# Kernel tuning notes

Measured on AMD Instinct MI355X. Metric: run time of the kernel, lower is better.

Reference implementation:

```python
import jax, jax.numpy as jnp
import numpy as np

B, S, H, P = 4, 4096, 1024, 10

def setup_inputs() -> dict:
    key = jax.random.key(0)
    k1, k2, k3, k4, k5 = jax.random.split(key, 5)
    return {
        "query": jax.random.normal(k1, (B, S, H), dtype=jnp.float32),
        "key": jax.random.normal(k2, (B, S, H), dtype=jnp.float32),
        "value": jax.random.normal(k3, (B, S, H), dtype=jnp.float32),
        "prefix_k": jax.random.normal(k4, (P, H), dtype=jnp.float32),
        "prefix_v": jax.random.normal(k5, (P, H), dtype=jnp.float32),
    }

def reference(query, key, value, prefix_k, prefix_v):
    # Broadcast learned prefix over batch and concat ahead of real K/V.
    b = query.shape[0]
    pk = jnp.broadcast_to(prefix_k[None], (b,) + prefix_k.shape)  # [B, P, H]
    pv = jnp.broadcast_to(prefix_v[None], (b,) + prefix_v.shape)
    k_all = jnp.concatenate([pk, key], axis=1)    # [B, P+S, H]
    v_all = jnp.concatenate([pv, value], axis=1)  # [B, P+S, H]
    # Raw (unscaled, unmasked) attention, exactly as the torch module does.
    scores = jnp.einsum("bqh,bkh->bqk", query, k_all)  # [B, S, P+S]
    attn = jax.nn.softmax(scores, axis=-1)
    return jnp.einsum("bqk,bkh->bqh", attn, v_all)     # [B, S, H]
```

## Files before the change

kernel.cpp:

```cpp
#include <hip/hip_runtime.h>
#include <cstdint>
#include <cstddef>

#define BB 4
#define SS 4096
#define HH 1024
#define PP 10
#define LL 4106
#define NTILES 129
#define CHUNKS_PB (NTILES * 4096)
#define TILE_ELEMS (4096 * 8)
#define LOG2E 1.44269504088896f

typedef __attribute__((ext_vector_type(8))) _Float16 half8v;
typedef __attribute__((ext_vector_type(4))) float float4v;

union hu16 { _Float16 h; unsigned short u; };

__device__ __forceinline__ half8v cvt8h(float4v f0, float4v f1) {
  half8v h;
  h[0] = (_Float16)f0[0]; h[1] = (_Float16)f0[1];
  h[2] = (_Float16)f0[2]; h[3] = (_Float16)f0[3];
  h[4] = (_Float16)f1[0]; h[5] = (_Float16)f1[1];
  h[6] = (_Float16)f1[2]; h[7] = (_Float16)f1[3];
  return h;
}
__device__ __forceinline__ unsigned pack2h(float a, float b) {
  hu16 x, y; x.h = (_Float16)a; y.h = (_Float16)b;
  return (unsigned)x.u | ((unsigned)y.u << 16);
}

template<int C>
__device__ __forceinline__ float dppf(float x) {
  return __int_as_float(
      __builtin_amdgcn_update_dpp(0, __float_as_int(x), C, 0xF, 0xF, true));
}
__device__ __forceinline__ float row16_max(float x) {
  x = fmaxf(x, dppf<0xB1>(x));
  x = fmaxf(x, dppf<0x4E>(x));
  x = fmaxf(x, dppf<0x140>(x));
  x = fmaxf(x, dppf<0x141>(x));
  return x;
}
__device__ __forceinline__ float row16_sum(float x) {
  x += dppf<0xB1>(x);
  x += dppf<0x4E>(x);
  x += dppf<0x140>(x);
  x += dppf<0x141>(x);
  return x;
}

#define LGKM_BAR() do { \
  asm volatile("s_waitcnt lgkmcnt(0)" ::: "memory"); \
  __builtin_amdgcn_s_barrier(); \
  asm volatile("" ::: "memory"); } while (0)

__global__ __launch_bounds__(256) void conv_k(const float* __restrict__ prefix_k,
                                              const float* __restrict__ key,
                                              _Float16* __restrict__ kp) {
  const int b = blockIdx.y;
  const int id = blockIdx.x * 256 + threadIdx.x;
  const int li = id & 15, g = (id >> 4) & 3, ktp = (id >> 6) & 31,
            nt = (id >> 11) & 1, it = id >> 12;
  const int n = it * 32 + nt * 16 + li;
  const int d = ktp * 32 + g * 8;
  float4v f0 = {0.f, 0.f, 0.f, 0.f}, f1 = {0.f, 0.f, 0.f, 0.f};
  if (n < LL) {
    const float* src = (n < PP) ? prefix_k + (size_t)n * HH + d
                                : key + ((size_t)b * SS + (n - PP)) * HH + d;
    f0 = *(const float4v*)src; f1 = *(const float4v*)(src + 4);
  }
  *(half8v*)(kp + ((size_t)b * CHUNKS_PB + id) * 8) = cvt8h(f0, f1);
}

__global__ __launch_bounds__(256) void conv_v(const float* __restrict__ prefix_v,
                                              const float* __restrict__ value,
                                              _Float16* __restrict__ vp) {
  const int b = blockIdx.y;
  const int id = blockIdx.x * 256 + threadIdx.x;
  const int d = id & 1023, g = (id >> 10) & 3, it = id >> 12;
  const int nb = it * 32 + g * 8;
  half8v h;
  #pragma unroll
  for (int j = 0; j < 8; ++j) {
    int n = nb + j;
    float f = 0.f;
    if (n < LL)
      f = (n < PP) ? prefix_v[(size_t)n * HH + d]
                   : value[((size_t)b * SS + (n - PP)) * HH + d];
    h[j] = (_Float16)f;
  }
  *(half8v*)(vp + ((size_t)b * CHUNKS_PB + id) * 8) = h;
}

template<int PATH>
__global__ __launch_bounds__(512, 2) void attn_fused(
    const float* __restrict__ q,
    const float* __restrict__ key,
    const float* __restrict__ value,
    const float* __restrict__ prefix_k,
    const float* __restrict__ prefix_v,
    const _Float16* __restrict__ kp,
    const _Float16* __restrict__ vp,
    float* __restrict__ out)
{
  __shared__ __align__(16) float sbuf0[8][32][36];
  __shared__ __align__(16) float sbuf1[8][32][36];
  __shared__ __align__(16) unsigned short Pl0[32][40];
  __shared__ __align__(16) unsigned short Pl1[32][40];
  __shared__ float sc0[32], sc1[32];
  __shared__ float l_l[32];

  const int tid = threadIdx.x;
  const int w = tid >> 6, ln = tid & 63, g = ln >> 4, li = ln & 15;
  const int bid = blockIdx.x, xcd = bid & 7, b = xcd >> 1;
  const int qt = ((bid >> 3) << 1) | (xcd & 1);
  const int q0 = qt * 32;
  const int dbase = w * 128;

  half8v qf[2][4];
  #pragma unroll
  for (int mt = 0; mt < 2; ++mt)
    #pragma unroll
    for (int kt = 0; kt < 4; ++kt) {
      const float* p = q + ((size_t)(b * SS + q0 + mt * 16 + li)) * HH + dbase + kt * 32 + g * 8;
      qf[mt][kt] = cvt8h(*(const float4v*)p, *(const float4v*)(p + 4));
    }

  float4v z4 = {0.f, 0.f, 0.f, 0.f};
  float4v o[2][8];
  #pragma unroll
  for (int mt = 0; mt < 2; ++mt)
    #pragma unroll
    for (int dt = 0; dt < 8; ++dt) o[mt][dt] = z4;
  float m_r = -1e30f, l_r = 0.f;

  const _Float16* kbase = kp + ((size_t)b * CHUNKS_PB + (size_t)(w * 4) * 64 + g * 16 + li) * 8;
  const _Float16* vbase = vp + ((size_t)b * CHUNKS_PB + (size_t)g * 1024 + dbase + li) * 8;

  half8v kreg[8];
  half8v vreg[8];
  if constexpr (PATH == 0) {
    #pragma unroll
    for (int kt = 0; kt < 4; ++kt)
      #pragma unroll
      for (int nt = 0; nt < 2; ++nt)
        kreg[kt * 2 + nt] = *(const half8v*)(kbase + (size_t)(nt * 2048 + kt * 64) * 8);
  }

  const int srow = w * 4 + (ln >> 4);
  const int c0 = (ln & 15) * 2;

  auto do_qk = [&](int i, float (*sb)[32][36]) __attribute__((always_inline)) {
    float4v sacc[2][2];
    sacc[0][0] = z4; sacc[0][1] = z4; sacc[1][0] = z4; sacc[1][1] = z4;
    #pragma unroll
    for (int kt = 0; kt < 4; ++kt) {
      half8v kb[2];
      if constexpr (PATH == 0) {
        kb[0] = kreg[kt * 2 + 0]; kb[1] = kreg[kt * 2 + 1];
      } else {
        #pragma unroll
        for (int nt = 0; nt < 2; ++nt) {
          int n = i * 32 + nt * 16 + li;
          int nc = (n < LL) ? n : 0;
          const float* kpp = (nc < PP) ? (prefix_k + (size_t)nc * HH)
                                       : (key + ((size_t)b * SS + (nc - PP)) * HH);
          kpp += dbase + kt * 32 + g * 8;
          kb[nt] = cvt8h(*(const float4v*)kpp, *(const float4v*)(kpp + 4));
        }
      }
      #pragma unroll
      for (int mt = 0; mt < 2; ++mt)
        #pragma unroll
        for (int nt = 0; nt < 2; ++nt)
          sacc[mt][nt] = __builtin_amdgcn_mfma_f32_16x16x32_f16(qf[mt][kt], kb[nt], sacc[mt][nt], 0, 0, 0);
    }
    #pragma unroll
    for (int mt = 0; mt < 2; ++mt)
      #pragma unroll
      for (int nt = 0; nt < 2; ++nt)
        #pragma unroll
        for (int r = 0; r < 4; ++r)
          sb[w][mt * 16 + g * 4 + r][nt * 16 + li] = sacc[mt][nt][r];
    if constexpr (PATH == 0) {
      kbase += TILE_ELEMS;
      #pragma unroll
      for (int kt = 0; kt < 4; ++kt)
        #pragma unroll
        for (int nt = 0; nt < 2; ++nt)
          kreg[kt * 2 + nt] = *(const half8v*)(kbase + (size_t)(nt * 2048 + kt * 64) * 8);
    }
  };

  auto do_softmax = [&](int t, const float (*sb)[32][36],
                        unsigned short (*plw)[40], float* scw)
      __attribute__((always_inline)) {
    float s0 = 0.f, s1 = 0.f;
    #pragma unroll
    for (int bw = 0; bw < 8; ++bw) {
      float2 tv = *(const float2*)&sb[bw][srow][c0];
      s0 += tv.x; s1 += tv.y;
    }
    if constexpr (PATH == 1) {
      if (t * 32 + c0 >= LL)     s0 = -1e30f;
      if (t * 32 + c0 + 1 >= LL) s1 = -1e30f;
    }
    const float mx = row16_max(fmaxf(s0, s1));
    const float m_new = fmaxf(m_r, mx);
    const float scp = exp2f((m_r - m_new) * LOG2E);
    const float p0 = exp2f((s0 - m_new) * LOG2E);
    const float p1 = exp2f((s1 - m_new) * LOG2E);
    const float ts = row16_sum(p0 + p1);
    l_r = l_r * scp + ts;
    m_r = m_new;
    *(unsigned*)&plw[srow][c0] = pack2h(p0, p1);
    if ((ln & 15) == 0) scw[srow] = scp;
  };

  auto do_pv = [&](int t, const unsigned short (*plr)[40], const float* scr)
      __attribute__((always_inline)) {
    float scc[2][4];
    #pragma unroll
    for (int mt = 0; mt < 2; ++mt)
      #pragma unroll
      for (int r = 0; r < 4; ++r)
        scc[mt][r] = scr[mt * 16 + g * 4 + r];
    #pragma unroll
    for (int mt = 0; mt < 2; ++mt)
      #pragma unroll
      for (int dt = 0; dt < 8; ++dt)
        #pragma unroll
        for (int r = 0; r < 4; ++r)
          o[mt][dt][r] *= scc[mt][r];
    half8v pa0 = *(const half8v*)&plr[li][g * 8];
    half8v pa1 = *(const half8v*)&plr[16 + li][g * 8];
    #pragma unroll
    for (int dt = 0; dt < 8; ++dt) {
      half8v vb;
      if constexpr (PATH == 0) {
        vb = vreg[dt];
      } else {
        const int d = dbase + dt * 16 + li;
        #pragma unroll
        for (int j = 0; j < 8; ++j) {
          int n = t * 32 + g * 8 + j;
          int nc = (n < LL) ? n : 0;
          float f = (nc < PP) ? prefix_v[(size_t)nc * HH + d]
                              : value[((size_t)b * SS + (nc - PP)) * HH + d];
          vb[j] = (_Float16)f;
        }
      }
      o[0][dt] = __builtin_amdgcn_mfma_f32_16x16x32_f16(pa0, vb, o[0][dt], 0, 0, 0);
      o[1][dt] = __builtin_amdgcn_mfma_f32_16x16x32_f16(pa1, vb, o[1][dt], 0, 0, 0);
    }
  };

  auto load_v = [&]() __attribute__((always_inline)) {
    if constexpr (PATH == 0) {
      #pragma unroll
      for (int dt = 0; dt < 8; ++dt)
        vreg[dt] = *(const half8v*)(vbase + (size_t)(dt * 16) * 8);
      vbase += TILE_ELEMS;
    }
  };

  do_qk(0, sbuf0);
  LGKM_BAR();
  do_qk(1, sbuf1); do_softmax(0, sbuf0, Pl0, sc0); load_v();
  LGKM_BAR();
  int i = 2;
  for (; i + 1 < NTILES; i += 2) {
    do_qk(i, sbuf0);
    do_pv(i - 2, Pl0, sc0);
    do_softmax(i - 1, sbuf1, Pl1, sc1);
    load_v();
    LGKM_BAR();
    do_qk(i + 1, sbuf1);
    do_pv(i - 1, Pl1, sc1);
    do_softmax(i, sbuf0, Pl0, sc0);
    load_v();
    LGKM_BAR();
  }
  do_qk(NTILES - 1, sbuf0);
  do_pv(NTILES - 3, Pl0, sc0);
  do_softmax(NTILES - 2, sbuf1, Pl1, sc1);
  load_v();
  LGKM_BAR();
  do_pv(NTILES - 2, Pl1, sc1);
  do_softmax(NTILES - 1, sbuf0, Pl0, sc0);
  load_v();
  LGKM_BAR();
  do_pv(NTILES - 1, Pl0, sc0);

  if ((ln & 15) == 0) l_l[srow] = l_r;
  LGKM_BAR();
  float il[2][4];
  #pragma unroll
  for (int mt = 0; mt < 2; ++mt)
    #pragma unroll
    for (int r = 0; r < 4; ++r)
      il[mt][r] = 1.0f / l_l[mt * 16 + g * 4 + r];
  #pragma unroll
  for (int mt = 0; mt < 2; ++mt)
    #pragma unroll
    for (int dt = 0; dt < 8; ++dt)
      #pragma unroll
      for (int r = 0; r < 4; ++r)
        out[((size_t)(b * SS + q0 + mt * 16 + g * 4 + r)) * HH + dbase + dt * 16 + li]
            = o[mt][dt][r] * il[mt][r];
}

extern "C" void kernel_launch(void* const* d_in, const int* in_sizes, int n_in,
                              void* d_out, int out_size, void* d_ws, size_t ws_size,
                              hipStream_t stream) {
  const float* q        = (const float*)d_in[0];
  const float* key      = (const float*)d_in[1];
  const float* value    = (const float*)d_in[2];
  const float* prefix_k = (const float*)d_in[3];
  const float* prefix_v = (const float*)d_in[4];
  float* out = (float*)d_out;

  const size_t PLANE = (size_t)BB * CHUNKS_PB * 8;
  const size_t NEED  = 2 * PLANE * sizeof(unsigned short);

  if (ws_size >= NEED) {
    _Float16* kp = (_Float16*)d_ws;
    _Float16* vp = kp + PLANE;
    conv_k<<<dim3(CHUNKS_PB / 256, BB), 256, 0, stream>>>(prefix_k, key, kp);
    conv_v<<<dim3(CHUNKS_PB / 256, BB), 256, 0, stream>>>(prefix_v, value, vp);
    attn_fused<0><<<512, 512, 0, stream>>>(q, key, value, prefix_k, prefix_v, kp, vp, out);
  } else {
    attn_fused<1><<<512, 512, 0, stream>>>(q, key, value, prefix_k, prefix_v,
                                           nullptr, nullptr, out);
  }
}
```

Baseline: 416.4 us.

## Process two 32-row query tiles per block to reuse loaded K/V fragments

Each block now handles 64 query rows as two independent 32-row sub-tiles (A and B), each with its own scores, softmax state and output accumulators. The K and V fp16 fragments loaded into registers are shared by both sub-tiles, halving global K/V traffic per query row, and the grid shrinks from 512 to 256 blocks. Score buffers change padding from 36 to 33. The costs are doubled register pressure from a second set of Q fragments and accumulators under launch_bounds(512,2), more LDS, and only 256 blocks on the device, which may underfill CUs or cause spills.

```diff
diff --git a/kernel.cpp b/kernel.cpp
--- a/kernel.cpp
+++ b/kernel.cpp
@@ -104,54 +104,70 @@
     const _Float16* __restrict__ vp,
     float* __restrict__ out)
 {
-  __shared__ __align__(16) float sbuf0[8][32][36];
-  __shared__ __align__(16) float sbuf1[8][32][36];
-  __shared__ __align__(16) unsigned short Pl0[32][40];
-  __shared__ __align__(16) unsigned short Pl1[32][40];
-  __shared__ float sc0[32], sc1[32];
-  __shared__ float l_l[32];
+  __shared__ __align__(16) float sbA0[8][32][33], sbA1[8][32][33];
+  __shared__ __align__(16) float sbB0[8][32][33], sbB1[8][32][33];
+  __shared__ __align__(16) unsigned short PlA0[32][40], PlA1[32][40];
+  __shared__ __align__(16) unsigned short PlB0[32][40], PlB1[32][40];
+  __shared__ float scA0[32], scA1[32], scB0[32], scB1[32];
+  __shared__ float lA[32], lB[32];
 
   const int tid = threadIdx.x;
   const int w = tid >> 6, ln = tid & 63, g = ln >> 4, li = ln & 15;
   const int bid = blockIdx.x, xcd = bid & 7, b = xcd >> 1;
   const int qt = ((bid >> 3) << 1) | (xcd & 1);
-  const int q0 = qt * 32;
+  const int q0 = qt * 64;
   const int dbase = w * 128;
 
-  half8v qf[2][4];
+  half8v qfA[2][4], qfB[2][4];
   #pragma unroll
   for (int mt = 0; mt < 2; ++mt)
     #pragma unroll
     for (int kt = 0; kt < 4; ++kt) {
-      const float* p = q + ((size_t)(b * SS + q0 + mt * 16 + li)) * HH + dbase + kt * 32 + g * 8;
-      qf[mt][kt] = cvt8h(*(const float4v*)p, *(const float4v*)(p + 4));
+      const float* pA = q + ((size_t)(b * SS + q0 + mt * 16 + li)) * HH + dbase + kt * 32 + g * 8;
+      const float* pB = pA + (size_t)32 * HH;
+      qfA[mt][kt] = cvt8h(*(const float4v*)pA, *(const float4v*)(pA + 4));
+      qfB[mt][kt] = cvt8h(*(const float4v*)pB, *(const float4v*)(pB + 4));
     }
 
   float4v z4 = {0.f, 0.f, 0.f, 0.f};
-  float4v o[2][8];
+  float4v oA[2][8], oB[2][8];
   #pragma unroll
   for (int mt = 0; mt < 2; ++mt)
     #pragma unroll
-    for (int dt = 0; dt < 8; ++dt) o[mt][dt] = z4;
-  float m_r = -1e30f, l_r = 0.f;
+    for (int dt = 0; dt < 8; ++dt) { oA[mt][dt] = z4; oB[mt][dt] = z4; }
+  float m_rA = -1e30f, l_rA = 0.f, m_rB = -1e30f, l_rB = 0.f;
 
   const _Float16* kbase = kp + ((size_t)b * CHUNKS_PB + (size_t)(w * 4) * 64 + g * 16 + li) * 8;
   const _Float16* vbase = vp + ((size_t)b * CHUNKS_PB + (size_t)g * 1024 + dbase + li) * 8;
 
   half8v kreg[8];
   half8v vreg[8];
-  if constexpr (PATH == 0) {
-    #pragma unroll
-    for (int kt = 0; kt < 4; ++kt)
-      #pragma unroll
-      for (int nt = 0; nt < 2; ++nt)
-        kreg[kt * 2 + nt] = *(const half8v*)(kbase + (size_t)(nt * 2048 + kt * 64) * 8);
-  }
 
   const int srow = w * 4 + (ln >> 4);
   const int c0 = (ln & 15) * 2;
 
-  auto do_qk = [&](int i, float (*sb)[32][36]) __attribute__((always_inline)) {
+  auto kload = [&]() __attribute__((always_inline)) {
+    if constexpr (PATH == 0) {
+      #pragma unroll
+      for (int kt = 0; kt < 4; ++kt)
+        #pragma unroll
+        for (int nt = 0; nt < 2; ++nt)
+          kreg[kt * 2 + nt] = *(const half8v*)(kbase + (size_t)(nt * 2048 + kt * 64) * 8);
+      kbase += TILE_ELEMS;
+    }
+  };
+
+  auto vload = [&]() __attribute__((always_inline)) {
+    if constexpr (PATH == 0) {
+      #pragma unroll
+      for (int dt = 0; dt < 8; ++dt)
+        vreg[dt] = *(const half8v*)(vbase + (size_t)(dt * 16) * 8);
+      vbase += TILE_ELEMS;
+    }
+  };
+
+  auto do_qk = [&](int i, const half8v (&qf)[2][4], float (*sb)[32][33])
+      __attribute__((always_inline)) {
     float4v sacc[2][2];
     sacc[0][0] = z4; sacc[0][1] = z4; sacc[1][0] = z4; sacc[1][1] = z4;
     #pragma unroll
@@ -183,18 +199,10 @@
         #pragma unroll
         for (int r = 0; r < 4; ++r)
           sb[w][mt * 16 + g * 4 + r][nt * 16 + li] = sacc[mt][nt][r];
-    if constexpr (PATH == 0) {
-      kbase += TILE_ELEMS;
-      #pragma unroll
-      for (int kt = 0; kt < 4; ++kt)
-        #pragma unroll
-        for (int nt = 0; nt < 2; ++nt)
-          kreg[kt * 2 + nt] = *(const half8v*)(kbase + (size_t)(nt * 2048 + kt * 64) * 8);
-    }
-  };
-
-  auto do_softmax = [&](int t, const float (*sb)[32][36],
-                        unsigned short (*plw)[40], float* scw)
+  };
+
+  auto do_sm = [&](int t, const float (*sb)[32][33],
+                   unsigned short (*plw)[40], float* scw, float& m_r, float& l_r)
       __attribute__((always_inline)) {
     float s0 = 0.f, s1 = 0.f;
     #pragma unroll
@@ -218,8 +226,8 @@
     if ((ln & 15) == 0) scw[srow] = scp;
   };
 
-  auto do_pv = [&](int t, const unsigned short (*plr)[40], const float* scr)
-      __attribute__((always_inline)) {
+  auto do_pv = [&](int t, const unsigned short (*plr)[40], const float* scr,
+                   float4v (&o)[2][8]) __attribute__((always_inline)) {
     float scc[2][4];
     #pragma unroll
     for (int mt = 0; mt < 2; ++mt)
@@ -256,59 +264,62 @@
     }
   };
 
-  auto load_v = [&]() __attribute__((always_inline)) {
-    if constexpr (PATH == 0) {
-      #pragma unroll
-      for (int dt = 0; dt < 8; ++dt)
-        vreg[dt] = *(const half8v*)(vbase + (size_t)(dt * 16) * 8);
-      vbase += TILE_ELEMS;
-    }
-  };
-
-  do_qk(0, sbuf0);
-  LGKM_BAR();
-  do_qk(1, sbuf1); do_softmax(0, sbuf0, Pl0, sc0); load_v();
+  kload();
+  do_qk(0, qfA, sbA0); do_qk(0, qfB, sbB0); kload();
+  LGKM_BAR();
+  do_qk(1, qfA, sbA1); do_qk(1, qfB, sbB1); kload();
+  do_sm(0, sbA0, PlA0, scA0, m_rA, l_rA);
+  do_sm(0, sbB0, PlB0, scB0, m_rB, l_rB);
+  vload();
   LGKM_BAR();
   int i = 2;
   for (; i + 1 < NTILES; i += 2) {
-    do_qk(i, sbuf0);
-    do_pv(i - 2, Pl0, sc0);
-    do_softmax(i - 1, sbuf1, Pl1, sc1);
-    load_v();
+    do_qk(i, qfA, sbA0); do_qk(i, qfB, sbB0); kload();
+    do_pv(i - 2, PlA0, scA0, oA); do_pv(i - 2, PlB0, scB0, oB);
+    do_sm(i - 1, sbA1, PlA1, scA1, m_rA, l_rA);
+    do_sm(i - 1, sbB1, PlB1, scB1, m_rB, l_rB);
+    vload();
     LGKM_BAR();
-    do_qk(i + 1, sbuf1);
-    do_pv(i - 1, Pl1, sc1);
-    do_softmax(i, sbuf0, Pl0, sc0);
-    load_v();
+    do_qk(i + 1, qfA, sbA1); do_qk(i + 1, qfB, sbB1); kload();
+    do_pv(i - 1, PlA1, scA1, oA); do_pv(i - 1, PlB1, scB1, oB);
+    do_sm(i, sbA0, PlA0, scA0, m_rA, l_rA);
+    do_sm(i, sbB0, PlB0, scB0, m_rB, l_rB);
+    vload();
     LGKM_BAR();
   }
-  do_qk(NTILES - 1, sbuf0);
-  do_pv(NTILES - 3, Pl0, sc0);
-  do_softmax(NTILES - 2, sbuf1, Pl1, sc1);
-  load_v();
-  LGKM_BAR();
-  do_pv(NTILES - 2, Pl1, sc1);
-  do_softmax(NTILES - 1, sbuf0, Pl0, sc0);
-  load_v();
-  LGKM_BAR();
-  do_pv(NTILES - 1, Pl0, sc0);
-
-  if ((ln & 15) == 0) l_l[srow] = l_r;
-  LGKM_BAR();
-  float il[2][4];
+  do_qk(NTILES - 1, qfA, sbA0); do_qk(NTILES - 1, qfB, sbB0);
+  do_pv(NTILES - 3, PlA0, scA0, oA); do_pv(NTILES - 3, PlB0, scB0, oB);
+  do_sm(NTILES - 2, sbA1, PlA1, scA1, m_rA, l_rA);
+  do_sm(NTILES - 2, sbB1, PlB1, scB1, m_rB, l_rB);
+  vload();
+  LGKM_BAR();
+  do_pv(NTILES - 2, PlA1, scA1, oA); do_pv(NTILES - 2, PlB1, scB1, oB);
+  do_sm(NTILES - 1, sbA0, PlA0, scA0, m_rA, l_rA);
+  do_sm(NTILES - 1, sbB0, PlB0, scB0, m_rB, l_rB);
+  vload();
+  LGKM_BAR();
+  do_pv(NTILES - 1, PlA0, scA0, oA); do_pv(NTILES - 1, PlB0, scB0, oB);
+
+  if ((ln & 15) == 0) { lA[srow] = l_rA; lB[srow] = l_rB; }
+  LGKM_BAR();
+  float ilA[2][4], ilB[2][4];
   #pragma unroll
   for (int mt = 0; mt < 2; ++mt)
     #pragma unroll
-    for (int r = 0; r < 4; ++r)
-      il[mt][r] = 1.0f / l_l[mt * 16 + g * 4 + r];
+    for (int r = 0; r < 4; ++r) {
+      ilA[mt][r] = 1.0f / lA[mt * 16 + g * 4 + r];
+      ilB[mt][r] = 1.0f / lB[mt * 16 + g * 4 + r];
+    }
   #pragma unroll
   for (int mt = 0; mt < 2; ++mt)
     #pragma unroll
     for (int dt = 0; dt < 8; ++dt)
       #pragma unroll
-      for (int r = 0; r < 4; ++r)
-        out[((size_t)(b * SS + q0 + mt * 16 + g * 4 + r)) * HH + dbase + dt * 16 + li]
-            = o[mt][dt][r] * il[mt][r];
+      for (int r = 0; r < 4; ++r) {
+        const size_t rowA = (size_t)(b * SS + q0 + mt * 16 + g * 4 + r);
+        out[rowA * HH + dbase + dt * 16 + li] = oA[mt][dt][r] * ilA[mt][r];
+        out[(rowA + 32) * HH + dbase + dt * 16 + li] = oB[mt][dt][r] * ilB[mt][r];
+      }
 }
 
 extern "C" void kernel_launch(void* const* d_in, const int* in_sizes, int n_in,
@@ -329,9 +340,9 @@
     _Float16* vp = kp + PLANE;
     conv_k<<<dim3(CHUNKS_PB / 256, BB), 256, 0, stream>>>(prefix_k, key, kp);
     conv_v<<<dim3(CHUNKS_PB / 256, BB), 256, 0, stream>>>(prefix_v, value, vp);
-    attn_fused<0><<<512, 512, 0, stream>>>(q, key, value, prefix_k, prefix_v, kp, vp, out);
+    attn_fused<0><<<256, 512, 0, stream>>>(q, key, value, prefix_k, prefix_v, kp, vp, out);
   } else {
-    attn_fused<1><<<512, 512, 0, stream>>>(q, key, value, prefix_k, prefix_v,
+    attn_fused<1><<<256, 512, 0, stream>>>(q, key, value, prefix_k, prefix_v,
                                            nullptr, nullptr, out);
   }
 }
```

Result: slower. 1.183 ms (+184.1%).

## Split head dimension across 16 waves per block instead of 8

Applied to the files above, without the earlier changes.

Doubles the block size to 1024 threads so each wave owns 64 head-dim columns instead of 128, halving per-wave K/V/Q register fragments and accumulators. The QK partial-score reduction now sums 16 wave slices in LDS, and softmax maps one thread per score element with a 32-lane reduction that adds a cross-row shuffle. The aim is more latency hiding through more waves and lower register pressure, at the cost of a larger shared-memory reduction, heavier barriers across 16 waves, and more LDS traffic per tile.

```diff
diff --git a/kernel.cpp b/kernel.cpp
--- a/kernel.cpp
+++ b/kernel.cpp
@@ -25,28 +25,26 @@
   h[6] = (_Float16)f1[2]; h[7] = (_Float16)f1[3];
   return h;
 }
-__device__ __forceinline__ unsigned pack2h(float a, float b) {
-  hu16 x, y; x.h = (_Float16)a; y.h = (_Float16)b;
-  return (unsigned)x.u | ((unsigned)y.u << 16);
-}
 
 template<int C>
 __device__ __forceinline__ float dppf(float x) {
   return __int_as_float(
       __builtin_amdgcn_update_dpp(0, __float_as_int(x), C, 0xF, 0xF, true));
 }
-__device__ __forceinline__ float row16_max(float x) {
+__device__ __forceinline__ float row32_max(float x) {
   x = fmaxf(x, dppf<0xB1>(x));
   x = fmaxf(x, dppf<0x4E>(x));
   x = fmaxf(x, dppf<0x140>(x));
   x = fmaxf(x, dppf<0x141>(x));
+  x = fmaxf(x, __shfl_xor(x, 16));
   return x;
 }
-__device__ __forceinline__ float row16_sum(float x) {
+__device__ __forceinline__ float row32_sum(float x) {
   x += dppf<0xB1>(x);
   x += dppf<0x4E>(x);
   x += dppf<0x140>(x);
   x += dppf<0x141>(x);
+  x += __shfl_xor(x, 16);
   return x;
 }
 
@@ -94,7 +92,7 @@
 }
 
 template<int PATH>
-__global__ __launch_bounds__(512, 2) void attn_fused(
+__global__ __launch_bounds__(1024, 4) void attn_fused(
     const float* __restrict__ q,
     const float* __restrict__ key,
     const float* __restrict__ value,
@@ -104,61 +102,64 @@
     const _Float16* __restrict__ vp,
     float* __restrict__ out)
 {
-  __shared__ __align__(16) float sbuf0[8][32][36];
-  __shared__ __align__(16) float sbuf1[8][32][36];
+  __shared__ __align__(16) float sbuf0[16][32][33];
+  __shared__ __align__(16) float sbuf1[16][32][33];
   __shared__ __align__(16) unsigned short Pl0[32][40];
   __shared__ __align__(16) unsigned short Pl1[32][40];
   __shared__ float sc0[32], sc1[32];
   __shared__ float l_l[32];
 
   const int tid = threadIdx.x;
-  const int w = tid >> 6, ln = tid & 63, g = ln >> 4, li = ln & 15;
+  const int w = tid >> 6, ln = tid & 63, g = (ln >> 4) & 3, li = ln & 15;
   const int bid = blockIdx.x, xcd = bid & 7, b = xcd >> 1;
   const int qt = ((bid >> 3) << 1) | (xcd & 1);
   const int q0 = qt * 32;
-  const int dbase = w * 128;
-
-  half8v qf[2][4];
+  const int dbase = w * 64;
+
+  half8v qf[2][2];
   #pragma unroll
   for (int mt = 0; mt < 2; ++mt)
     #pragma unroll
-    for (int kt = 0; kt < 4; ++kt) {
+    for (int kt = 0; kt < 2; ++kt) {
       const float* p = q + ((size_t)(b * SS + q0 + mt * 16 + li)) * HH + dbase + kt * 32 + g * 8;
       qf[mt][kt] = cvt8h(*(const float4v*)p, *(const float4v*)(p + 4));
     }
 
   float4v z4 = {0.f, 0.f, 0.f, 0.f};
-  float4v o[2][8];
+  float4v o[2][4];
   #pragma unroll
   for (int mt = 0; mt < 2; ++mt)
     #pragma unroll
-    for (int dt = 0; dt < 8; ++dt) o[mt][dt] = z4;
+    for (int dt = 0; dt < 4; ++dt) o[mt][dt] = z4;
   float m_r = -1e30f, l_r = 0.f;
 
-  const _Float16* kbase = kp + ((size_t)b * CHUNKS_PB + (size_t)(w * 4) * 64 + g * 16 + li) * 8;
-  const _Float16* vbase = vp + ((size_t)b * CHUNKS_PB + (size_t)g * 1024 + dbase + li) * 8;
-
-  half8v kreg[8];
-  half8v vreg[8];
+  const _Float16* kbase = kp + (size_t)b * CHUNKS_PB * 8
+                          + (size_t)(w * 2) * 512 + (g * 16 + li) * 8;
+  const _Float16* vbase = vp + (size_t)b * CHUNKS_PB * 8
+                          + (size_t)g * 8192 + (size_t)(dbase + li) * 8;
+
+  half8v kreg[2][2];
+  half8v vreg[4];
   if constexpr (PATH == 0) {
     #pragma unroll
-    for (int kt = 0; kt < 4; ++kt)
-      #pragma unroll
-      for (int nt = 0; nt < 2; ++nt)
-        kreg[kt * 2 + nt] = *(const half8v*)(kbase + (size_t)(nt * 2048 + kt * 64) * 8);
-  }
-
-  const int srow = w * 4 + (ln >> 4);
-  const int c0 = (ln & 15) * 2;
-
-  auto do_qk = [&](int i, float (*sb)[32][36]) __attribute__((always_inline)) {
+    for (int nt = 0; nt < 2; ++nt)
+      #pragma unroll
+      for (int kt = 0; kt < 2; ++kt)
+        kreg[nt][kt] = *(const half8v*)(kbase + nt * 16384 + kt * 512);
+    kbase += TILE_ELEMS;
+  }
+
+  const int srow = tid >> 5;
+  const int scol = tid & 31;
+
+  auto do_qk = [&](int i, float (*sb)[32][33]) __attribute__((always_inline)) {
     float4v sacc[2][2];
     sacc[0][0] = z4; sacc[0][1] = z4; sacc[1][0] = z4; sacc[1][1] = z4;
     #pragma unroll
-    for (int kt = 0; kt < 4; ++kt) {
+    for (int kt = 0; kt < 2; ++kt) {
       half8v kb[2];
       if constexpr (PATH == 0) {
-        kb[0] = kreg[kt * 2 + 0]; kb[1] = kreg[kt * 2 + 1];
+        kb[0] = kreg[0][kt]; kb[1] = kreg[1][kt];
       } else {
         #pragma unroll
         for (int nt = 0; nt < 2; ++nt) {
@@ -184,38 +185,34 @@
         for (int r = 0; r < 4; ++r)
           sb[w][mt * 16 + g * 4 + r][nt * 16 + li] = sacc[mt][nt][r];
     if constexpr (PATH == 0) {
+      #pragma unroll
+      for (int nt = 0; nt < 2; ++nt)
+        #pragma unroll
+        for (int kt = 0; kt < 2; ++kt)
+          kreg[nt][kt] = *(const half8v*)(kbase + nt * 16384 + kt * 512);
       kbase += TILE_ELEMS;
-      #pragma unroll
-      for (int kt = 0; kt < 4; ++kt)
-        #pragma unroll
-        for (int nt = 0; nt < 2; ++nt)
-          kreg[kt * 2 + nt] = *(const half8v*)(kbase + (size_t)(nt * 2048 + kt * 64) * 8);
     }
   };
 
-  auto do_softmax = [&](int t, const float (*sb)[32][36],
-                        unsigned short (*plw)[40], float* scw)
+  auto do_sm = [&](int t, const float (*sb)[32][33],
+                   unsigned short (*plw)[40], float* scw)
       __attribute__((always_inline)) {
-    float s0 = 0.f, s1 = 0.f;
-    #pragma unroll
-    for (int bw = 0; bw < 8; ++bw) {
-      float2 tv = *(const float2*)&sb[bw][srow][c0];
-      s0 += tv.x; s1 += tv.y;
-    }
+    float s = 0.f;
+    #pragma unroll
+    for (int i = 0; i < 16; ++i) s += sb[i][srow][scol];
     if constexpr (PATH == 1) {
-      if (t * 32 + c0 >= LL)     s0 = -1e30f;
-      if (t * 32 + c0 + 1 >= LL) s1 = -1e30f;
-    }
-    const float mx = row16_max(fmaxf(s0, s1));
+      if (t * 32 + scol >= LL) s = -1e30f;
+    }
+    const float mx = row32_max(s);
     const float m_new = fmaxf(m_r, mx);
     const float scp = exp2f((m_r - m_new) * LOG2E);
-    const float p0 = exp2f((s0 - m_new) * LOG2E);
-    const float p1 = exp2f((s1 - m_new) * LOG2E);
-    const float ts = row16_sum(p0 + p1);
+    const float p = exp2f((s - m_new) * LOG2E);
+    const float ts = row32_sum(p);
     l_r = l_r * scp + ts;
     m_r = m_new;
-    *(unsigned*)&plw[srow][c0] = pack2h(p0, p1);
-    if ((ln & 15) == 0) scw[srow] = scp;
+    hu16 hp; hp.h = (_Float16)p;
+    plw[srow][scol] = hp.u;
+    if (scol == 0) scw[srow] = scp;
   };
 
   auto do_pv = [&](int t, const unsigned short (*plr)[40], const float* scr)
@@ -229,14 +226,14 @@
     #pragma unroll
     for (int mt = 0; mt < 2; ++mt)
       #pragma unroll
-      for (int dt = 0; dt < 8; ++dt)
+      for (int dt = 0; dt < 4; ++dt)
         #pragma unroll
         for (int r = 0; r < 4; ++r)
           o[mt][dt][r] *= scc[mt][r];
     half8v pa0 = *(const half8v*)&plr[li][g * 8];
     half8v pa1 = *(const half8v*)&plr[16 + li][g * 8];
     #pragma unroll
-    for (int dt = 0; dt < 8; ++dt) {
+    for (int dt = 0; dt < 4; ++dt) {
       half8v vb;
       if constexpr (PATH == 0) {
         vb = vreg[dt];
@@ -259,41 +256,41 @@
   auto load_v = [&]() __attribute__((always_inline)) {
     if constexpr (PATH == 0) {
       #pragma unroll
-      for (int dt = 0; dt < 8; ++dt)
-        vreg[dt] = *(const half8v*)(vbase + (size_t)(dt * 16) * 8);
+      for (int dt = 0; dt < 4; ++dt)
+        vreg[dt] = *(const half8v*)(vbase + dt * 128);
       vbase += TILE_ELEMS;
     }
   };
 
   do_qk(0, sbuf0);
   LGKM_BAR();
-  do_qk(1, sbuf1); do_softmax(0, sbuf0, Pl0, sc0); load_v();
+  do_qk(1, sbuf1); do_sm(0, sbuf0, Pl0, sc0); load_v();
   LGKM_BAR();
   int i = 2;
   for (; i + 1 < NTILES; i += 2) {
     do_qk(i, sbuf0);
     do_pv(i - 2, Pl0, sc0);
-    do_softmax(i - 1, sbuf1, Pl1, sc1);
+    do_sm(i - 1, sbuf1, Pl1, sc1);
     load_v();
     LGKM_BAR();
     do_qk(i + 1, sbuf1);
     do_pv(i - 1, Pl1, sc1);
-    do_softmax(i, sbuf0, Pl0, sc0);
+    do_sm(i, sbuf0, Pl0, sc0);
     load_v();
     LGKM_BAR();
   }
   do_qk(NTILES - 1, sbuf0);
   do_pv(NTILES - 3, Pl0, sc0);
-  do_softmax(NTILES - 2, sbuf1, Pl1, sc1);
+  do_sm(NTILES - 2, sbuf1, Pl1, sc1);
   load_v();
   LGKM_BAR();
   do_pv(NTILES - 2, Pl1, sc1);
-  do_softmax(NTILES - 1, sbuf0, Pl0, sc0);
+  do_sm(NTILES - 1, sbuf0, Pl0, sc0);
   load_v();
   LGKM_BAR();
   do_pv(NTILES - 1, Pl0, sc0);
 
-  if ((ln & 15) == 0) l_l[srow] = l_r;
+  if (scol == 0) l_l[srow] = l_r;
   LGKM_BAR();
   float il[2][4];
   #pragma unroll
@@ -304,7 +301,7 @@
   #pragma unroll
   for (int mt = 0; mt < 2; ++mt)
     #pragma unroll
-    for (int dt = 0; dt < 8; ++dt)
+    for (int dt = 0; dt < 4; ++dt)
       #pragma unroll
       for (int r = 0; r < 4; ++r)
         out[((size_t)(b * SS + q0 + mt * 16 + g * 4 + r)) * HH + dbase + dt * 16 + li]
@@ -329,9 +326,9 @@
     _Float16* vp = kp + PLANE;
     conv_k<<<dim3(CHUNKS_PB / 256, BB), 256, 0, stream>>>(prefix_k, key, kp);
     conv_v<<<dim3(CHUNKS_PB / 256, BB), 256, 0, stream>>>(prefix_v, value, vp);
-    attn_fused<0><<<512, 512, 0, stream>>>(q, key, value, prefix_k, prefix_v, kp, vp, out);
+    attn_fused<0><<<512, 1024, 0, stream>>>(q, key, value, prefix_k, prefix_v, kp, vp, out);
   } else {
-    attn_fused<1><<<512, 512, 0, stream>>>(q, key, value, prefix_k, prefix_v,
-                                           nullptr, nullptr, out);
-  }
-}
+    attn_fused<1><<<512, 1024, 0, stream>>>(q, key, value, prefix_k, prefix_v,
+                                            nullptr, nullptr, out);
+  }
+}
```

New measurement: 590.3 us. +41.8%, slower.
